# Kernel optimization log

Hardware: AMD Instinct MI355X
Metric: run time of the kernel (lower is better)

## Reference

```python
import jax, jax.numpy as jnp
import numpy as np

B, S, D, H = 4, 2048, 1024, 16
HD = D // H  # head_dim = 64


def setup_inputs() -> dict:
    key = jax.random.key(0)
    ks = jax.random.split(key, 9)
    sc = 1.0 / np.sqrt(D)
    return {
        "x": jax.random.normal(ks[0], (B, S, D), dtype=jnp.float32),
        "Wq": jax.random.normal(ks[1], (D, D), dtype=jnp.float32) * sc,
        "bq": jnp.zeros((D,), dtype=jnp.float32),
        "Wk": jax.random.normal(ks[2], (D, D), dtype=jnp.float32) * sc,
        "bk": jnp.zeros((D,), dtype=jnp.float32),
        "Wv": jax.random.normal(ks[3], (D, D), dtype=jnp.float32) * sc,
        "bv": jnp.zeros((D,), dtype=jnp.float32),
        "Wo": jax.random.normal(ks[4], (D, D), dtype=jnp.float32) * sc,
        "bo": jnp.zeros((D,), dtype=jnp.float32),
    }


def reference(x, Wq, bq, Wk, bk, Wv, bv, Wo, bo):
    # QKV projections (torch Linear: x @ W.T + b), reshape to [B, H, S, HD]
    def proj(W, b):
        return (x @ W.T + b).reshape(B, S, H, HD).transpose(0, 2, 1, 3)

    Q, K, V = proj(Wq, bq), proj(Wk, bk), proj(Wv, bv)
    scores = jnp.einsum("bhqd,bhkd->bhqk", Q, K) / jnp.sqrt(jnp.float32(HD))
    attn = jax.nn.softmax(scores, axis=-1)  # dropout is identity at eval
    ctx = jnp.einsum("bhqk,bhkd->bhqd", attn, V)
    ctx = ctx.transpose(0, 2, 1, 3).reshape(B, S, D)
    out = ctx @ Wo.T + bo
    return out, attn
```

## Files before the change

### kernel.cpp

```cpp
#include <hip/hip_runtime.h>
#include <stdint.h>

#define Mm 8192
#define Dd 1024

typedef unsigned short u16;
typedef __attribute__((ext_vector_type(8))) short bf16x8;
typedef __attribute__((ext_vector_type(4))) float f32x4;
typedef __attribute__((ext_vector_type(4))) u16 u16x4;

__device__ __forceinline__ u16 f2bf(float f) {
  union { float f; uint32_t u; } c; c.f = f;
  uint32_t u = c.u;
  return (u16)((u + 0x7fffu + ((u >> 16) & 1u)) >> 16);
}

__device__ __forceinline__ float EXP2(float x) {
#if __has_builtin(__builtin_amdgcn_exp2f)
  return __builtin_amdgcn_exp2f(x);
#else
  return exp2f(x);
#endif
}

__device__ __forceinline__ float LOG2(float x) {
#if __has_builtin(__builtin_amdgcn_logf)
  return __builtin_amdgcn_logf(x);
#else
  return log2f(x);
#endif
}

__device__ __forceinline__ uint32_t cvtpk(float a, float b) {
  uint32_t r;
  asm("v_cvt_pk_bf16_f32 %0, %1, %2" : "=v"(r) : "v"(a), "v"(b));
  return r;
}

__device__ __forceinline__ void gll16(const void* g, void* l) {
  __builtin_amdgcn_global_load_lds((const __attribute__((address_space(1))) void*)g,
                                   (__attribute__((address_space(3))) void*)l, 16, 0, 0);
}

__global__ void cvt_all(const float* __restrict__ x, const float* __restrict__ wq,
                        const float* __restrict__ wk, const float* __restrict__ wv,
                        const float* __restrict__ wo, u16* __restrict__ out) {
  const int xn4 = 2097152, wn4 = 262144;
  const int total = xn4 + 4 * wn4;
  int i = blockIdx.x * blockDim.x + threadIdx.x;
  int stride = gridDim.x * blockDim.x;
  for (; i < total; i += stride) {
    const float* src; int off;
    if (i < xn4) { src = x; off = i; }
    else {
      int j = i - xn4; int wsel = j >> 18; off = j & (wn4 - 1);
      src = (wsel == 0) ? wq : (wsel == 1) ? wk : (wsel == 2) ? wv : wo;
    }
    float4 v = ((const float4*)src)[off];
    u16x4 o;
    o.x = f2bf(v.x); o.y = f2bf(v.y); o.z = f2bf(v.z); o.w = f2bf(v.w);
    ((u16x4*)out)[i] = o;
  }
}

__global__ __launch_bounds__(256) void gemm_qkv(
    const u16* __restrict__ A, const u16* __restrict__ Wt,
    const float* __restrict__ bq, const float* __restrict__ bk, const float* __restrict__ bv,
    u16* __restrict__ Qo, u16* __restrict__ Ko, u16* __restrict__ Vo, float qscale)
{
  __shared__ u16 As[128 * 32];
  __shared__ u16 Bs[128 * 32];
  const int K = 1024, tiles_n = 24;
  int nwg = 64 * 24;
  int bid = blockIdx.x;
  { int q = nwg >> 3; bid = (bid & 7) * q + (bid >> 3); }
  int tm = bid / tiles_n, tn = bid % tiles_n;
  int tid = threadIdx.x;
  int wid = tid >> 6, lane = tid & 63;
  int wr = wid >> 1, wc = wid & 1;

  f32x4 acc[4][4] = {};
  int a_row = wr * 64 + (lane & 15);
  int b_row = wc * 64 + (lane & 15);
  int frag_k = (lane >> 4) * 8;

  const u16* ga0 = A + (size_t)(tm * 128 + wid * 32 + (lane >> 2)) * K + (lane & 3) * 8;
  const u16* ga1 = ga0 + (size_t)16 * K;
  const u16* gb0 = Wt + (size_t)(tn * 128 + wid * 32 + (lane >> 2)) * K + (lane & 3) * 8;
  const u16* gb1 = gb0 + (size_t)16 * K;
  u16* lA0 = As + wid * 1024;
  u16* lA1 = As + wid * 1024 + 512;
  u16* lB0 = Bs + wid * 1024;
  u16* lB1 = Bs + wid * 1024 + 512;

  for (int kt = 0; kt < K; kt += 32) {
    gll16(ga0 + kt, lA0);
    gll16(ga1 + kt, lA1);
    gll16(gb0 + kt, lB0);
    gll16(gb1 + kt, lB1);
    __syncthreads();
    bf16x8 af[4], bfr[4];
#pragma unroll
    for (int i = 0; i < 4; i++)
      af[i] = *(const bf16x8*)(As + (a_row + i * 16) * 32 + frag_k);
#pragma unroll
    for (int i = 0; i < 4; i++)
      bfr[i] = *(const bf16x8*)(Bs + (b_row + i * 16) * 32 + frag_k);
#pragma unroll
    for (int i = 0; i < 4; i++)
#pragma unroll
      for (int j = 0; j < 4; j++)
        acc[i][j] = __builtin_amdgcn_mfma_f32_16x16x32_bf16(af[i], bfr[j], acc[i][j], 0, 0, 0);
    __syncthreads();
  }

#pragma unroll
  for (int i = 0; i < 4; i++) {
#pragma unroll
    for (int j = 0; j < 4; j++) {
      int col = tn * 128 + wc * 64 + j * 16 + (lane & 15);
      int wsel = col >> 10, c10 = col & 1023;
      int h = c10 >> 6, hd = c10 & 63;
      float bvv = (wsel == 0 ? bq : wsel == 1 ? bk : bv)[c10];
      int row0 = tm * 128 + wr * 64 + i * 16 + (lane >> 4) * 4;
      int b_ = row0 >> 11, s0 = row0 & 2047;
      if (wsel == 2) {
        u16x4 o;
#pragma unroll
        for (int r = 0; r < 4; r++) o[r] = f2bf(acc[i][j][r] + bvv);
        *(u16x4*)&Vo[((size_t)(b_ * 16 + h) * 64 + hd) * 2048 + s0] = o;
      } else {
        u16* dst = (wsel == 0) ? Qo : Ko;
        float sc = (wsel == 0) ? qscale : 1.0f;
#pragma unroll
        for (int r = 0; r < 4; r++)
          dst[(((size_t)(b_ * 16 + h) * 2048 + (s0 + r)) << 6) + hd] = f2bf((acc[i][j][r] + bvv) * sc);
      }
    }
  }
}

__global__ __launch_bounds__(256) void gemm_out(
    const u16* __restrict__ A, const u16* __restrict__ Bt,
    const float* __restrict__ bias, float* __restrict__ out,
    int M, int N, int K)
{
  __shared__ u16 As[128 * 32];
  __shared__ u16 Bs[128 * 32];
  int tiles_n = N >> 7;
  int nwg = (M >> 7) * tiles_n;
  int bid = blockIdx.x;
  { int q = nwg >> 3; bid = (bid & 7) * q + (bid >> 3); }
  int tm = bid / tiles_n, tn = bid % tiles_n;
  int tid = threadIdx.x;
  int wid = tid >> 6, lane = tid & 63;
  int wr = wid >> 1, wc = wid & 1;

  f32x4 acc[4][4] = {};
  int a_row = wr * 64 + (lane & 15);
  int b_row = wc * 64 + (lane & 15);
  int frag_k = (lane >> 4) * 8;

  const u16* ga0 = A + (size_t)(tm * 128 + wid * 32 + (lane >> 2)) * K + (lane & 3) * 8;
  const u16* ga1 = ga0 + (size_t)16 * K;
  const u16* gb0 = Bt + (size_t)(tn * 128 + wid * 32 + (lane >> 2)) * K + (lane & 3) * 8;
  const u16* gb1 = gb0 + (size_t)16 * K;
  u16* lA0 = As + wid * 1024;
  u16* lA1 = As + wid * 1024 + 512;
  u16* lB0 = Bs + wid * 1024;
  u16* lB1 = Bs + wid * 1024 + 512;

  for (int kt = 0; kt < K; kt += 32) {
    gll16(ga0 + kt, lA0);
    gll16(ga1 + kt, lA1);
    gll16(gb0 + kt, lB0);
    gll16(gb1 + kt, lB1);
    __syncthreads();
    bf16x8 af[4], bfr[4];
#pragma unroll
    for (int i = 0; i < 4; i++)
      af[i] = *(const bf16x8*)(As + (a_row + i * 16) * 32 + frag_k);
#pragma unroll
    for (int i = 0; i < 4; i++)
      bfr[i] = *(const bf16x8*)(Bs + (b_row + i * 16) * 32 + frag_k);
#pragma unroll
    for (int i = 0; i < 4; i++)
#pragma unroll
      for (int j = 0; j < 4; j++)
        acc[i][j] = __builtin_amdgcn_mfma_f32_16x16x32_bf16(af[i], bfr[j], acc[i][j], 0, 0, 0);
    __syncthreads();
  }

#pragma unroll
  for (int i = 0; i < 4; i++)
#pragma unroll
    for (int j = 0; j < 4; j++) {
      int col = tn * 128 + wc * 64 + j * 16 + (lane & 15);
      float bv = bias[col];
#pragma unroll
      for (int r = 0; r < 4; r++) {
        int row = tm * 128 + wr * 64 + i * 16 + (lane >> 4) * 4 + r;
        out[(size_t)row * N + col] = acc[i][j][r] + bv;
      }
    }
}

__global__ __launch_bounds__(512, 8) void attn_pass1(
    const u16* __restrict__ Qb, const u16* __restrict__ Kb, float* __restrict__ lrbuf)
{
  __shared__ u16 Ks[4][4096];
  int bid = blockIdx.x;
  int swz = (bid & 7) * 128 + (bid >> 3);
  int bh = swz >> 4, qt = swz & 15;
  int tid = threadIdx.x, w = tid >> 6, lane = tid & 63;
  int g = lane >> 4, l15 = lane & 15;

  const u16* Qg = Qb + ((size_t)bh * 2048 + qt * 128) * 64;
  const u16* Kg = Kb + (size_t)bh * 2048 * 64;
  int qloc = w * 16 + l15;
  bf16x8 aq0 = *(const bf16x8*)(Qg + (size_t)qloc * 64 + g * 8);
  bf16x8 aq1 = *(const bf16x8*)(Qg + (size_t)qloc * 64 + 32 + g * 8);

  int srow = w * 8 + (lane >> 3);
  int schunk = (lane & 7) ^ (lane >> 3);
  const u16* Ksrc = Kg + (size_t)srow * 64 + schunk * 8;

  float ls0 = 0.f, ls1 = 0.f, ls2 = 0.f, ls3 = 0.f;
  gll16(Ksrc, (char*)Ks[0] + w * 1024);
  gll16(Ksrc + 4096, (char*)Ks[1] + w * 1024);
  for (int it = 0; it < 32; ++it) {
    if (it < 30) gll16(Ksrc + (size_t)(it + 2) * 4096, (char*)Ks[(it + 2) & 3] + w * 1024);
    if (it < 30)       asm volatile("s_waitcnt vmcnt(2)" ::: "memory");
    else if (it == 30) asm volatile("s_waitcnt vmcnt(1)" ::: "memory");
    else               asm volatile("s_waitcnt vmcnt(0)" ::: "memory");
    __builtin_amdgcn_s_barrier();
    const char* Kbase = (const char*)Ks[it & 3];
    f32x4 s[4] = {};
    __builtin_amdgcn_s_setprio(1);
#pragma unroll
    for (int t = 0; t < 4; t++) {
      int kr = t * 16 + l15;
      int x = (kr & 7) << 4;
      bf16x8 k0 = *(const bf16x8*)(Kbase + kr * 128 + ((g * 16) ^ x));
      bf16x8 k1 = *(const bf16x8*)(Kbase + kr * 128 + ((64 + g * 16) ^ x));
      s[t] = __builtin_amdgcn_mfma_f32_16x16x32_bf16(k0, aq0, s[t], 0, 0, 0);
      s[t] = __builtin_amdgcn_mfma_f32_16x16x32_bf16(k1, aq1, s[t], 0, 0, 0);
    }
    __builtin_amdgcn_s_setprio(0);
#pragma unroll
    for (int r = 0; r < 4; r++) {
      ls0 += EXP2(s[0][r]); ls1 += EXP2(s[1][r]);
      ls2 += EXP2(s[2][r]); ls3 += EXP2(s[3][r]);
    }
  }
  float lsum = (ls0 + ls1) + (ls2 + ls3);
  lsum += __shfl_xor(lsum, 16);
  lsum += __shfl_xor(lsum, 32);
  if (!g) lrbuf[(size_t)bh * 2048 + qt * 128 + qloc] = -LOG2(lsum);
}

__global__ __launch_bounds__(512, 4) void attn_pass2(
    const u16* __restrict__ Qb, const u16* __restrict__ Kb,
    const u16* __restrict__ Vtb, const float* __restrict__ lrbuf,
    float* __restrict__ attn_out, u16* __restrict__ ctxb)
{
  __shared__ u16 Ks[4][4096];
  __shared__ u16 Vs[4][4096];
  __shared__ u16 Ps[8192];

  int bid = blockIdx.x;
  int swz = (bid & 7) * 128 + (bid >> 3);
  int bh = swz >> 4, qt = swz & 15;
  int tid = threadIdx.x, w = tid >> 6, lane = tid & 63;
  int g = lane >> 4, l15 = lane & 15;

  const u16* Qg = Qb + ((size_t)bh * 2048 + qt * 128) * 64;
  const u16* Kg = Kb + (size_t)bh * 2048 * 64;
  const u16* Vg = Vtb + (size_t)bh * 64 * 2048;
  float* Ag = attn_out + ((size_t)bh * 2048 + qt * 128) * 2048;

  int qloc = w * 16 + l15;
  bf16x8 aq0 = *(const bf16x8*)(Qg + (size_t)qloc * 64 + g * 8);
  bf16x8 aq1 = *(const bf16x8*)(Qg + (size_t)qloc * 64 + 32 + g * 8);
  float lr2 = lrbuf[(size_t)bh * 2048 + qt * 128 + qloc];

  int srow = w * 8 + (lane >> 3);
  int schunk = (lane & 7) ^ (lane >> 3);
  const u16* Ksrc = Kg + (size_t)srow * 64 + schunk * 8;
  const u16* Vsrc = Vg + (size_t)srow * 2048 + schunk * 8;

  int xq = (qloc & 7) << 4;
  char* Pb = (char*)Ps + qloc * 128;

  f32x4 ctx[4] = {};
#pragma unroll
  for (int p = 0; p < 2; p++) {
    gll16(Ksrc + (size_t)p * 4096, (char*)Ks[p] + w * 1024);
    gll16(Vsrc + (size_t)p * 64,  (char*)Vs[p] + w * 1024);
  }
  for (int it = 0; it < 32; ++it) {
    if (it < 30) {
      gll16(Ksrc + (size_t)(it + 2) * 4096, (char*)Ks[(it + 2) & 3] + w * 1024);
      gll16(Vsrc + (size_t)(it + 2) * 64,  (char*)Vs[(it + 2) & 3] + w * 1024);
    }
    if (it == 0)       asm volatile("s_waitcnt vmcnt(4)" ::: "memory");
    else if (it == 1)  asm volatile("s_waitcnt vmcnt(8)" ::: "memory");
    else if (it < 30)  asm volatile("s_waitcnt vmcnt(12)" ::: "memory");
    else if (it == 30) asm volatile("s_waitcnt vmcnt(10)" ::: "memory");
    else               asm volatile("s_waitcnt vmcnt(8)" ::: "memory");
    __builtin_amdgcn_s_barrier();
    const char* Kbase = (const char*)Ks[it & 3];
    const char* Vbase = (const char*)Vs[it & 3];
    f32x4 s[4] = {};
    __builtin_amdgcn_s_setprio(1);
#pragma unroll
    for (int t = 0; t < 4; t++) {
      int kr = t * 16 + l15;
      int x = (kr & 7) << 4;
      bf16x8 k0 = *(const bf16x8*)(Kbase + kr * 128 + ((g * 16) ^ x));
      bf16x8 k1 = *(const bf16x8*)(Kbase + kr * 128 + ((64 + g * 16) ^ x));
      s[t] = __builtin_amdgcn_mfma_f32_16x16x32_bf16(k0, aq0, s[t], 0, 0, 0);
      s[t] = __builtin_amdgcn_mfma_f32_16x16x32_bf16(k1, aq1, s[t], 0, 0, 0);
    }
    __builtin_amdgcn_s_setprio(0);
    float* Arow = Ag + (size_t)qloc * 2048 + it * 64 + g * 4;
#pragma unroll
    for (int t = 0; t < 4; t++) {
      f32x4 p;
#pragma unroll
      for (int r = 0; r < 4; r++) p[r] = EXP2(s[t][r] + lr2);
      __builtin_nontemporal_store(p, (f32x4*)(Arow + t * 16));
      uint2 pk;
      pk.x = cvtpk(p[0], p[1]);
      pk.y = cvtpk(p[2], p[3]);
      *(uint2*)(Pb + ((t * 32 + g * 8) ^ xq)) = pk;
    }
    __builtin_amdgcn_s_setprio(1);
#pragma unroll
    for (int kk = 0; kk < 2; kk++) {
      bf16x8 ap = *(const bf16x8*)(Pb + ((kk * 64 + g * 16) ^ xq));
#pragma unroll
      for (int t = 0; t < 4; t++) {
        int dr = t * 16 + l15;
        bf16x8 bv = *(const bf16x8*)(Vbase + dr * 128 + ((kk * 64 + g * 16) ^ ((dr & 7) << 4)));
        ctx[t] = __builtin_amdgcn_mfma_f32_16x16x32_bf16(ap, bv, ctx[t], 0, 0, 0);
      }
    }
    __builtin_amdgcn_s_setprio(0);
  }

  int b_ = bh >> 4, h = bh & 15;
#pragma unroll
  for (int t = 0; t < 4; t++)
#pragma unroll
    for (int r = 0; r < 4; r++) {
      int qg = qt * 128 + w * 16 + g * 4 + r;
      int col = h * 64 + t * 16 + l15;
      ctxb[((size_t)b_ * 2048 + qg) * 1024 + col] = f2bf(ctx[t][r]);
    }
}

extern "C" void kernel_launch(void* const* d_in, const int* in_sizes, int n_in,
                              void* d_out, int out_size, void* d_ws, size_t ws_size,
                              hipStream_t stream) {
  const float* x  = (const float*)d_in[0];
  const float* Wq = (const float*)d_in[1];
  const float* bq = (const float*)d_in[2];
  const float* Wk = (const float*)d_in[3];
  const float* bk = (const float*)d_in[4];
  const float* Wv = (const float*)d_in[5];
  const float* bv = (const float*)d_in[6];
  const float* Wo = (const float*)d_in[7];
  const float* bo = (const float*)d_in[8];

  u16* xb   = (u16*)d_ws;
  u16* Wqb  = xb + (size_t)Mm * Dd;
  u16* Wkb  = Wqb + (size_t)Dd * Dd;
  u16* Wvb  = Wkb + (size_t)Dd * Dd;
  u16* Wob  = Wvb + (size_t)Dd * Dd;
  u16* Qb   = Wob + (size_t)Dd * Dd;
  u16* Kbuf = Qb + (size_t)Mm * Dd;
  u16* Vtb  = Kbuf + (size_t)Mm * Dd;
  u16* ctxb = Vtb + (size_t)Mm * Dd;
  float* lrbuf = (float*)(ctxb + (size_t)Mm * Dd);

  float* out_f = (float*)d_out;
  float* attn_o = out_f + (size_t)Mm * Dd;

  cvt_all<<<2048, 256, 0, stream>>>(x, Wq, Wk, Wv, Wo, xb);

  const float qscale = 0.125f * 1.44269504088896340736f;
  gemm_qkv<<<1536, 256, 0, stream>>>(xb, Wqb, bq, bk, bv, Qb, Kbuf, Vtb, qscale);
  attn_pass1<<<1024, 512, 0, stream>>>(Qb, Kbuf, lrbuf);
  attn_pass2<<<1024, 512, 0, stream>>>(Qb, Kbuf, Vtb, lrbuf, attn_o, ctxb);
  gemm_out<<<512, 256, 0, stream>>>(ctxb, Wob, bo, out_f, Mm, Dd, Dd);
}
```

Before: 509.0 us.

## Fuse attention row-sum pass and softmax/PV pass into one kernel

Merges the two attention kernels into one. Each block first computes the softmax denominator over all K tiles, then recomputes the scores to write the attention probabilities and accumulate P·V. This removes a kernel launch, the lrbuf round trip and one reload of Q per block. Both phases share a single 8-slot LDS buffer, with deeper prefetch and larger K batches in phase one. In exchange, occupancy is limited to the pass2 level of 4 blocks for the whole kernel, and extra barriers are added for buffer reuse.

Result: faster. 436.6 us (median of 2 runs) (-14.2%).

```diff
diff --git a/kernel.cpp b/kernel.cpp
--- a/kernel.cpp
+++ b/kernel.cpp
@@ -205,10 +205,14 @@
     }
 }
 
-__global__ __launch_bounds__(512, 8) void attn_pass1(
-    const u16* __restrict__ Qb, const u16* __restrict__ Kb, float* __restrict__ lrbuf)
+__global__ __launch_bounds__(512, 4) void attn_fused(
+    const u16* __restrict__ Qb, const u16* __restrict__ Kb,
+    const u16* __restrict__ Vtb, float* __restrict__ attn_out,
+    u16* __restrict__ ctxb)
 {
-  __shared__ u16 Ks[4][4096];
+  __shared__ u16 Ks[8][4096];
+  __shared__ u16 Ps[8192];
+
   int bid = blockIdx.x;
   int swz = (bid & 7) * 128 + (bid >> 3);
   int bh = swz >> 4, qt = swz & 15;
@@ -217,6 +221,9 @@
 
   const u16* Qg = Qb + ((size_t)bh * 2048 + qt * 128) * 64;
   const u16* Kg = Kb + (size_t)bh * 2048 * 64;
+  const u16* Vg = Vtb + (size_t)bh * 64 * 2048;
+  float* Ag = attn_out + ((size_t)bh * 2048 + qt * 128) * 2048;
+
   int qloc = w * 16 + l15;
   bf16x8 aq0 = *(const bf16x8*)(Qg + (size_t)qloc * 64 + g * 8);
   bf16x8 aq1 = *(const bf16x8*)(Qg + (size_t)qloc * 64 + 32 + g * 8);
@@ -224,18 +231,73 @@
   int srow = w * 8 + (lane >> 3);
   int schunk = (lane & 7) ^ (lane >> 3);
   const u16* Ksrc = Kg + (size_t)srow * 64 + schunk * 8;
+  const u16* Vsrc = Vg + (size_t)srow * 2048 + schunk * 8;
 
   float ls0 = 0.f, ls1 = 0.f, ls2 = 0.f, ls3 = 0.f;
-  gll16(Ksrc, (char*)Ks[0] + w * 1024);
-  gll16(Ksrc + 4096, (char*)Ks[1] + w * 1024);
+#pragma unroll
+  for (int t = 0; t < 4; t++)
+    gll16(Ksrc + (size_t)t * 4096, (char*)Ks[t] + w * 1024);
+  for (int o = 0; o < 8; ++o) {
+    int gb = (o & 1) << 2;
+    if (o < 7) {
+#pragma unroll
+      for (int t = 0; t < 4; t++)
+        gll16(Ksrc + (size_t)(4 * o + 4 + t) * 4096, (char*)Ks[(gb ^ 4) + t] + w * 1024);
+      asm volatile("s_waitcnt vmcnt(4)" ::: "memory");
+    } else {
+      asm volatile("s_waitcnt vmcnt(0)" ::: "memory");
+    }
+    __builtin_amdgcn_s_barrier();
+#pragma unroll
+    for (int t4 = 0; t4 < 4; t4++) {
+      const char* Kbase = (const char*)Ks[gb + t4];
+      f32x4 s[4] = {};
+      __builtin_amdgcn_s_setprio(1);
+#pragma unroll
+      for (int t = 0; t < 4; t++) {
+        int kr = t * 16 + l15;
+        int x = (kr & 7) << 4;
+        bf16x8 k0 = *(const bf16x8*)(Kbase + kr * 128 + ((g * 16) ^ x));
+        bf16x8 k1 = *(const bf16x8*)(Kbase + kr * 128 + ((64 + g * 16) ^ x));
+        s[t] = __builtin_amdgcn_mfma_f32_16x16x32_bf16(k0, aq0, s[t], 0, 0, 0);
+        s[t] = __builtin_amdgcn_mfma_f32_16x16x32_bf16(k1, aq1, s[t], 0, 0, 0);
+      }
+      __builtin_amdgcn_s_setprio(0);
+#pragma unroll
+      for (int r = 0; r < 4; r++) {
+        ls0 += EXP2(s[0][r]); ls1 += EXP2(s[1][r]);
+        ls2 += EXP2(s[2][r]); ls3 += EXP2(s[3][r]);
+      }
+    }
+    asm volatile("" ::: "memory");
+    __builtin_amdgcn_s_barrier();
+  }
+  float lsum = (ls0 + ls1) + (ls2 + ls3);
+  lsum += __shfl_xor(lsum, 16);
+  lsum += __shfl_xor(lsum, 32);
+  float lr2 = -LOG2(lsum);
+
+  f32x4 ctx[4] = {};
+  int xq = (qloc & 7) << 4;
+  char* Pb = (char*)Ps + qloc * 128;
+#pragma unroll
+  for (int p = 0; p < 3; p++) {
+    gll16(Ksrc + (size_t)p * 4096, (char*)Ks[p] + w * 1024);
+    gll16(Vsrc + (size_t)p * 64,  (char*)Ks[4 + p] + w * 1024);
+  }
   for (int it = 0; it < 32; ++it) {
-    if (it < 30) gll16(Ksrc + (size_t)(it + 2) * 4096, (char*)Ks[(it + 2) & 3] + w * 1024);
-    if (it < 30)       asm volatile("s_waitcnt vmcnt(2)" ::: "memory");
-    else if (it == 30) asm volatile("s_waitcnt vmcnt(1)" ::: "memory");
-    else               asm volatile("s_waitcnt vmcnt(0)" ::: "memory");
+    int nx = (it + 3) & 31;
+    int nb = (it + 3) & 3;
+    gll16(Ksrc + (size_t)nx * 4096, (char*)Ks[nb] + w * 1024);
+    gll16(Vsrc + (size_t)nx * 64,  (char*)Ks[4 + nb] + w * 1024);
+    if (it == 0)      asm volatile("s_waitcnt vmcnt(6)" ::: "memory");
+    else if (it == 1) asm volatile("s_waitcnt vmcnt(10)" ::: "memory");
+    else if (it == 2) asm volatile("s_waitcnt vmcnt(14)" ::: "memory");
+    else              asm volatile("s_waitcnt vmcnt(18)" ::: "memory");
     __builtin_amdgcn_s_barrier();
+    f32x4 s[4] = {};
     const char* Kbase = (const char*)Ks[it & 3];
-    f32x4 s[4] = {};
+    const char* Vbase = (const char*)Ks[4 + (it & 3)];
     __builtin_amdgcn_s_setprio(1);
 #pragma unroll
     for (int t = 0; t < 4; t++) {
@@ -247,82 +309,6 @@
       s[t] = __builtin_amdgcn_mfma_f32_16x16x32_bf16(k1, aq1, s[t], 0, 0, 0);
     }
     __builtin_amdgcn_s_setprio(0);
-#pragma unroll
-    for (int r = 0; r < 4; r++) {
-      ls0 += EXP2(s[0][r]); ls1 += EXP2(s[1][r]);
-      ls2 += EXP2(s[2][r]); ls3 += EXP2(s[3][r]);
-    }
-  }
-  float lsum = (ls0 + ls1) + (ls2 + ls3);
-  lsum += __shfl_xor(lsum, 16);
-  lsum += __shfl_xor(lsum, 32);
-  if (!g) lrbuf[(size_t)bh * 2048 + qt * 128 + qloc] = -LOG2(lsum);
-}
-
-__global__ __launch_bounds__(512, 4) void attn_pass2(
-    const u16* __restrict__ Qb, const u16* __restrict__ Kb,
-    const u16* __restrict__ Vtb, const float* __restrict__ lrbuf,
-    float* __restrict__ attn_out, u16* __restrict__ ctxb)
-{
-  __shared__ u16 Ks[4][4096];
-  __shared__ u16 Vs[4][4096];
-  __shared__ u16 Ps[8192];
-
-  int bid = blockIdx.x;
-  int swz = (bid & 7) * 128 + (bid >> 3);
-  int bh = swz >> 4, qt = swz & 15;
-  int tid = threadIdx.x, w = tid >> 6, lane = tid & 63;
-  int g = lane >> 4, l15 = lane & 15;
-
-  const u16* Qg = Qb + ((size_t)bh * 2048 + qt * 128) * 64;
-  const u16* Kg = Kb + (size_t)bh * 2048 * 64;
-  const u16* Vg = Vtb + (size_t)bh * 64 * 2048;
-  float* Ag = attn_out + ((size_t)bh * 2048 + qt * 128) * 2048;
-
-  int qloc = w * 16 + l15;
-  bf16x8 aq0 = *(const bf16x8*)(Qg + (size_t)qloc * 64 + g * 8);
-  bf16x8 aq1 = *(const bf16x8*)(Qg + (size_t)qloc * 64 + 32 + g * 8);
-  float lr2 = lrbuf[(size_t)bh * 2048 + qt * 128 + qloc];
-
-  int srow = w * 8 + (lane >> 3);
-  int schunk = (lane & 7) ^ (lane >> 3);
-  const u16* Ksrc = Kg + (size_t)srow * 64 + schunk * 8;
-  const u16* Vsrc = Vg + (size_t)srow * 2048 + schunk * 8;
-
-  int xq = (qloc & 7) << 4;
-  char* Pb = (char*)Ps + qloc * 128;
-
-  f32x4 ctx[4] = {};
-#pragma unroll
-  for (int p = 0; p < 2; p++) {
-    gll16(Ksrc + (size_t)p * 4096, (char*)Ks[p] + w * 1024);
-    gll16(Vsrc + (size_t)p * 64,  (char*)Vs[p] + w * 1024);
-  }
-  for (int it = 0; it < 32; ++it) {
-    if (it < 30) {
-      gll16(Ksrc + (size_t)(it + 2) * 4096, (char*)Ks[(it + 2) & 3] + w * 1024);
-      gll16(Vsrc + (size_t)(it + 2) * 64,  (char*)Vs[(it + 2) & 3] + w * 1024);
-    }
-    if (it == 0)       asm volatile("s_waitcnt vmcnt(4)" ::: "memory");
-    else if (it == 1)  asm volatile("s_waitcnt vmcnt(8)" ::: "memory");
-    else if (it < 30)  asm volatile("s_waitcnt vmcnt(12)" ::: "memory");
-    else if (it == 30) asm volatile("s_waitcnt vmcnt(10)" ::: "memory");
-    else               asm volatile("s_waitcnt vmcnt(8)" ::: "memory");
-    __builtin_amdgcn_s_barrier();
-    const char* Kbase = (const char*)Ks[it & 3];
-    const char* Vbase = (const char*)Vs[it & 3];
-    f32x4 s[4] = {};
-    __builtin_amdgcn_s_setprio(1);
-#pragma unroll
-    for (int t = 0; t < 4; t++) {
-      int kr = t * 16 + l15;
-      int x = (kr & 7) << 4;
-      bf16x8 k0 = *(const bf16x8*)(Kbase + kr * 128 + ((g * 16) ^ x));
-      bf16x8 k1 = *(const bf16x8*)(Kbase + kr * 128 + ((64 + g * 16) ^ x));
-      s[t] = __builtin_amdgcn_mfma_f32_16x16x32_bf16(k0, aq0, s[t], 0, 0, 0);
-      s[t] = __builtin_amdgcn_mfma_f32_16x16x32_bf16(k1, aq1, s[t], 0, 0, 0);
-    }
-    __builtin_amdgcn_s_setprio(0);
     float* Arow = Ag + (size_t)qloc * 2048 + it * 64 + g * 4;
 #pragma unroll
     for (int t = 0; t < 4; t++) {
@@ -347,6 +333,8 @@
       }
     }
     __builtin_amdgcn_s_setprio(0);
+    asm volatile("" ::: "memory");
+    __builtin_amdgcn_s_barrier();
   }
 
   int b_ = bh >> 4, h = bh & 15;
@@ -382,7 +370,6 @@
   u16* Kbuf = Qb + (size_t)Mm * Dd;
   u16* Vtb  = Kbuf + (size_t)Mm * Dd;
   u16* ctxb = Vtb + (size_t)Mm * Dd;
-  float* lrbuf = (float*)(ctxb + (size_t)Mm * Dd);
 
   float* out_f = (float*)d_out;
   float* attn_o = out_f + (size_t)Mm * Dd;
@@ -391,7 +378,6 @@
 
   const float qscale = 0.125f * 1.44269504088896340736f;
   gemm_qkv<<<1536, 256, 0, stream>>>(xb, Wqb, bq, bk, bv, Qb, Kbuf, Vtb, qscale);
-  attn_pass1<<<1024, 512, 0, stream>>>(Qb, Kbuf, lrbuf);
-  attn_pass2<<<1024, 512, 0, stream>>>(Qb, Kbuf, Vtb, lrbuf, attn_o, ctxb);
+  attn_fused<<<1024, 512, 0, stream>>>(Qb, Kbuf, Vtb, attn_o, ctxb);
   gemm_out<<<512, 256, 0, stream>>>(ctxb, Wob, bo, out_f, Mm, Dd, Dd);
 }
```
